# Kernel optimization log

Measured on AMD Instinct MI355X. Metric: run time of the kernel, lower is better.

The kernel has to match this reference:

```python
import jax, jax.numpy as jnp
import numpy as np

N_NODES = 50000
N_EDGES = 1_600_000
D = 64


def setup_inputs() -> dict:
    key = jax.random.key(0)
    k1, k2, k3, k4 = jax.random.split(key, 4)
    x = jax.random.normal(k1, (N_NODES, D), dtype=jnp.float32)
    # Glorot-ish scale for the dense transform
    weight = jax.random.normal(k2, (D, D), dtype=jnp.float32) * (1.0 / np.sqrt(D))
    bias = jnp.zeros((D,), dtype=jnp.float32)
    src = jax.random.randint(k3, (N_EDGES,), 0, N_NODES, dtype=jnp.int32)
    dst = jax.random.randint(k4, (N_EDGES,), 0, N_NODES, dtype=jnp.int32)
    t = jnp.zeros((1,), dtype=jnp.float32)
    return {"t": t, "x": x, "weight": weight, "bias": bias, "src": src, "dst": dst}


def reference(t, x, weight, bias, src, dst):
    # GCDEFunc.forward(t, x) -> GCNLayer(x); dropout=0 (eval / ODE solve).
    n = x.shape[0]
    # symmetric GCN normalization: 1/sqrt(in_degree), 0 for isolated nodes
    deg = jax.ops.segment_sum(jnp.ones_like(dst, dtype=x.dtype), dst, num_segments=n)
    norm = jnp.where(deg > 0, jax.lax.rsqrt(jnp.maximum(deg, 1.0)), 0.0)[:, None]  # [N,1]
    h = x @ weight                 # [N,D] dense transform
    h = h * norm                   # src-side normalization
    # SpMM: sum messages copy_src(h) over incoming edges
    h = jax.ops.segment_sum(h[src], dst, num_segments=n)  # [N,D]
    h = h * norm + bias            # dst-side normalization + bias
    return jax.nn.softplus(h)      # smooth activation for ODE dynamics
```

## Files before the change

### kernel.cpp

```cpp
#include <hip/hip_runtime.h>
#include <hip/hip_fp16.h>

constexpr int N = 50000;
constexpr int D = 64;
constexpr int E = 1600000;
constexpr int NBUCK = (N + 127) / 128;
constexpr int CAP = 4608;
constexpr int BTHREADS = 512;
constexpr int BBLOCKS = 512;
constexpr int EPB = E / BBLOCKS;
constexpr int CPT = (EPB + BTHREADS - 1) / BTHREADS;

__global__ void k_init(int* __restrict__ cursor) {
    int t = threadIdx.x;
    if (t < NBUCK) cursor[t] = t * CAP;
}

__global__ void k_bucket(const int* __restrict__ src, const int* __restrict__ dst,
                         int* __restrict__ cursor, unsigned* __restrict__ packed) {
    __shared__ int lh[NBUCK];
    __shared__ int scanI[NBUCK];
    __shared__ int wsum[8];
    __shared__ int lb[NBUCK];
    __shared__ unsigned stage[EPB];
    int tid = threadIdx.x;
    if (tid < NBUCK) lh[tid] = 0;
    __syncthreads();
    int base_e = blockIdx.x * EPB;
    unsigned pk[CPT];
    int bn[CPT], rk[CPT];
#pragma unroll
    for (int i = 0; i < CPT; ++i) {
        int idx = i * BTHREADS + tid;
        if (idx < EPB) {
            int e = base_e + idx;
            int d = dst[e];
            int s = src[e];
            bn[i] = d >> 7;
            pk[i] = ((unsigned)d << 16) | (unsigned)s;
            rk[i] = atomicAdd(&lh[bn[i]], 1);
        } else bn[i] = -1;
    }
    __syncthreads();
    int w = tid >> 6, l = tid & 63;
    int v = (tid < NBUCK) ? lh[tid] : 0;
    for (int off = 1; off < 64; off <<= 1) {
        int t = __shfl_up(v, off, 64);
        if (l >= off) v += t;
    }
    if (tid < NBUCK) scanI[tid] = v;
    if (l == 63) wsum[w] = v;
    __syncthreads();
    if (tid < 64) {
        int s = (tid < 8) ? wsum[tid] : 0;
        for (int off = 1; off < 8; off <<= 1) {
            int t = __shfl_up(s, off, 64);
            if (tid >= off) s += t;
        }
        if (tid < 8) wsum[tid] = s;
    }
    __syncthreads();
    if (tid < NBUCK && w > 0) scanI[tid] += wsum[w - 1];
    if (tid < NBUCK) {
        int c = lh[tid];
        lb[tid] = c ? atomicAdd(&cursor[tid], c) : 0;
    }
    __syncthreads();
#pragma unroll
    for (int i = 0; i < CPT; ++i) {
        if (bn[i] >= 0) {
            int eb = (bn[i] == 0) ? 0 : scanI[bn[i] - 1];
            stage[eb + rk[i]] = pk[i];
        }
    }
    __syncthreads();
    for (int j = tid; j < EPB; j += BTHREADS) {
        unsigned vv = stage[j];
        int bk = vv >> 23;
        int eb = (bk == 0) ? 0 : scanI[bk - 1];
        packed[lb[bk] + (j - eb)] = vv;
    }
}

__global__ void k_csr(const int* __restrict__ cursor, const unsigned* __restrict__ packed,
                      unsigned short* __restrict__ csr, int* __restrict__ rowptr,
                      int* __restrict__ rowend, float* __restrict__ norm) {
    __shared__ int cnt[128];
    __shared__ int sm[128];
    __shared__ int cur[128];
    __shared__ unsigned short stage[CAP];
    int b = blockIdx.x, tid = threadIdx.x;
    if (tid < 128) cnt[tid] = 0;
    __syncthreads();
    int beg = b * CAP;
    int m = cursor[b] - beg;
    for (int j = tid; j < m; j += 1024)
        atomicAdd(&cnt[(packed[beg + j] >> 16) & 127], 1);
    __syncthreads();
    if (tid < 64) {
        int a = cnt[2 * tid], c1 = cnt[2 * tid + 1];
        int s = a + c1;
        for (int off = 1; off < 64; off <<= 1) {
            int t = __shfl_up(s, off, 64);
            if (tid >= off) s += t;
        }
        sm[2 * tid + 1] = s;
        sm[2 * tid] = s - c1;
    }
    __syncthreads();
    if (tid < 128) {
        int incl = sm[tid];
        int excl = incl - cnt[tid];
        int node = b * 128 + tid;
        if (node < N) {
            rowptr[node] = beg + excl;
            rowend[node] = beg + incl;
            norm[node] = cnt[tid] ? rsqrtf((float)cnt[tid]) : 0.0f;
        }
        cur[tid] = excl;
    }
    __syncthreads();
    for (int j = tid; j < m; j += 1024) {
        unsigned p = packed[beg + j];
        int slot = atomicAdd(&cur[(p >> 16) & 127], 1);
        stage[slot] = (unsigned short)(p & 0xFFFFu);
    }
    __syncthreads();
    unsigned* du = (unsigned*)(csr + beg);
    const unsigned* su = (const unsigned*)stage;
    int mu = m >> 1;
    for (int k = tid; k < mu; k += 1024) du[k] = su[k];
    if ((m & 1) && tid == 0) csr[beg + m - 1] = stage[m - 1];
}

__global__ void k_gemm(const float* __restrict__ x, const float* __restrict__ W,
                       const float* __restrict__ norm, __half* __restrict__ h2) {
    __shared__ float Wl[64 * 64];
    __shared__ float xs[16][64];
    int tid = threadIdx.x;
    const float4* W4 = (const float4*)W;
    float4* Wl4 = (float4*)Wl;
    Wl4[tid] = W4[tid];
    int r = tid >> 6, d = tid & 63;
    int row = blockIdx.x * 16 + r;
    xs[r][d] = x[row * 64 + d];
    __syncthreads();
    float a = 0.0f;
#pragma unroll
    for (int k = 0; k < 64; ++k) a = fmaf(xs[r][k], Wl[k * 64 + d], a);
    h2[row * 64 + d] = __float2half(a * norm[row]);
}

__global__ void k_aggregate(const int* __restrict__ rowptr, const int* __restrict__ rowend,
                            const unsigned short* __restrict__ csr,
                            const __half* __restrict__ h2, const float* __restrict__ norm,
                            const float* __restrict__ bias, float* __restrict__ out) {
    int node = blockIdx.x * 4 + (threadIdx.x >> 6);
    int lane = threadIdx.x & 63;
    int half = lane >> 5;
    int fl = lane & 31;
    const __half2* h2v = (const __half2*)h2;
    int beg = rowptr[node];
    int end = rowend[node];
    int deg = end - beg;
    int myidx = (beg + lane < end) ? (int)csr[beg + lane] : 0;
    int window = deg < 64 ? deg : 64;
    int npair = window >> 1;
    float ax = 0.0f, ay = 0.0f, bx = 0.0f, by = 0.0f;
    int p = 0;
    for (; p + 3 < npair; p += 4) {
        int s0 = __shfl(myidx, 2 * p + half, 64);
        int s1 = __shfl(myidx, 2 * p + 2 + half, 64);
        int s2 = __shfl(myidx, 2 * p + 4 + half, 64);
        int s3 = __shfl(myidx, 2 * p + 6 + half, 64);
        float2 v0 = __half22float2(h2v[s0 * 32 + fl]);
        float2 v1 = __half22float2(h2v[s1 * 32 + fl]);
        float2 v2 = __half22float2(h2v[s2 * 32 + fl]);
        float2 v3 = __half22float2(h2v[s3 * 32 + fl]);
        ax += v0.x + v2.x;  ay += v0.y + v2.y;
        bx += v1.x + v3.x;  by += v1.y + v3.y;
    }
    for (; p < npair; ++p) {
        int s = __shfl(myidx, 2 * p + half, 64);
        float2 v = __half22float2(h2v[s * 32 + fl]);
        ax += v.x;  ay += v.y;
    }
    if (window & 1) {
        int s = __shfl(myidx, window - 1, 64);
        float2 v = __half22float2(h2v[s * 32 + fl]);
        if (half == 0) { ax += v.x;  ay += v.y; }
    }
    if (deg > 64) {
        int j = beg + 64;
        for (; j + 1 < end; j += 2) {
            int s = csr[j + half];
            float2 v = __half22float2(h2v[s * 32 + fl]);
            ax += v.x;  ay += v.y;
        }
        if (j < end) {
            int s = csr[j];
            float2 v = __half22float2(h2v[s * 32 + fl]);
            if (half == 0) { ax += v.x;  ay += v.y; }
        }
    }
    ax += bx;  ay += by;
    ax += __shfl_xor(ax, 32, 64);
    ay += __shfl_xor(ay, 32, 64);
    if (half == 0) {
        float nrm = norm[node];
        float2 bs = ((const float2*)bias)[fl];
        float vx = ax * nrm + bs.x;
        float vy = ay * nrm + bs.y;
        float2 o;
        o.x = fmaxf(vx, 0.0f) + log1pf(expf(-fabsf(vx)));
        o.y = fmaxf(vy, 0.0f) + log1pf(expf(-fabsf(vy)));
        ((float2*)out)[node * 32 + fl] = o;
    }
}

extern "C" void kernel_launch(void* const* d_in, const int* in_sizes, int n_in,
                              void* d_out, int out_size, void* d_ws, size_t ws_size,
                              hipStream_t stream) {
    const float* x    = (const float*)d_in[1];
    const float* W    = (const float*)d_in[2];
    const float* bias = (const float*)d_in[3];
    const int* src = (const int*)d_in[4];
    const int* dst = (const int*)d_in[5];
    float* out = (float*)d_out;

    char* ws = (char*)d_ws;
    __half*         h2     = (__half*)(ws);
    unsigned*       packed = (unsigned*)(ws + 6400000);
    unsigned short* csr    = (unsigned short*)(ws + 13606912);
    int*            rowptr = (int*)(ws + 17210368);
    int*            rowend = (int*)(ws + 17410368);
    float*          norm   = (float*)(ws + 17610368);
    int*            cursor = (int*)(ws + 17810368);

    k_init     <<<1, 512, 0, stream>>>(cursor);
    k_bucket   <<<BBLOCKS, BTHREADS, 0, stream>>>(src, dst, cursor, packed);
    k_csr      <<<NBUCK, 1024, 0, stream>>>(cursor, packed, csr, rowptr, rowend, norm);
    k_gemm     <<<(N + 15) / 16, 1024, 0, stream>>>(x, W, norm, h2);
    k_aggregate<<<(N + 3) / 4, 256, 0, stream>>>(rowptr, rowend, csr, h2, norm, bias, out);
}
```

Measured before the change: 161.5 us.

## Replace init kernel with memset, persistent GEMM blocks, deeper gather unroll

The cursor initialization kernel is replaced by a memset, with bucket offsets made relative so the base is added in the bucket kernel. The GEMM becomes a grid-stride loop over 256 blocks, so W is loaded into shared memory once per block instead of once per 16 rows. The aggregation loop is unrolled to eight gathers per iteration to put more loads in flight. These are three unrelated tweaks. The memset may cost about as much as the tiny kernel it replaces, and fewer GEMM blocks lowers parallelism.

```diff
diff --git a/kernel.cpp b/kernel.cpp
--- a/kernel.cpp
+++ b/kernel.cpp
@@ -10,11 +10,6 @@
 constexpr int BBLOCKS = 512;
 constexpr int EPB = E / BBLOCKS;
 constexpr int CPT = (EPB + BTHREADS - 1) / BTHREADS;
-
-__global__ void k_init(int* __restrict__ cursor) {
-    int t = threadIdx.x;
-    if (t < NBUCK) cursor[t] = t * CAP;
-}
 
 __global__ void k_bucket(const int* __restrict__ src, const int* __restrict__ dst,
                          int* __restrict__ cursor, unsigned* __restrict__ packed) {
@@ -63,7 +58,7 @@
     if (tid < NBUCK && w > 0) scanI[tid] += wsum[w - 1];
     if (tid < NBUCK) {
         int c = lh[tid];
-        lb[tid] = c ? atomicAdd(&cursor[tid], c) : 0;
+        lb[tid] = tid * CAP + (c ? atomicAdd(&cursor[tid], c) : 0);
     }
     __syncthreads();
 #pragma unroll
@@ -93,7 +88,7 @@
     if (tid < 128) cnt[tid] = 0;
     __syncthreads();
     int beg = b * CAP;
-    int m = cursor[b] - beg;
+    int m = cursor[b];
     for (int j = tid; j < m; j += 1024)
         atomicAdd(&cnt[(packed[beg + j] >> 16) & 127], 1);
     __syncthreads();
@@ -138,17 +133,18 @@
     __shared__ float Wl[64 * 64];
     __shared__ float xs[16][64];
     int tid = threadIdx.x;
-    const float4* W4 = (const float4*)W;
-    float4* Wl4 = (float4*)Wl;
-    Wl4[tid] = W4[tid];
+    ((float4*)Wl)[tid] = ((const float4*)W)[tid];
     int r = tid >> 6, d = tid & 63;
-    int row = blockIdx.x * 16 + r;
-    xs[r][d] = x[row * 64 + d];
-    __syncthreads();
-    float a = 0.0f;
+    for (int tile = blockIdx.x; tile < N / 16; tile += 256) {
+        int row = tile * 16 + r;
+        __syncthreads();
+        xs[r][d] = x[row * 64 + d];
+        __syncthreads();
+        float a = 0.0f;
 #pragma unroll
-    for (int k = 0; k < 64; ++k) a = fmaf(xs[r][k], Wl[k * 64 + d], a);
-    h2[row * 64 + d] = __float2half(a * norm[row]);
+        for (int k = 0; k < 64; ++k) a = fmaf(xs[r][k], Wl[k * 64 + d], a);
+        h2[row * 64 + d] = __float2half(a * norm[row]);
+    }
 }
 
 __global__ void k_aggregate(const int* __restrict__ rowptr, const int* __restrict__ rowend,
@@ -168,17 +164,25 @@
     int npair = window >> 1;
     float ax = 0.0f, ay = 0.0f, bx = 0.0f, by = 0.0f;
     int p = 0;
-    for (; p + 3 < npair; p += 4) {
+    for (; p + 7 < npair; p += 8) {
         int s0 = __shfl(myidx, 2 * p + half, 64);
         int s1 = __shfl(myidx, 2 * p + 2 + half, 64);
         int s2 = __shfl(myidx, 2 * p + 4 + half, 64);
         int s3 = __shfl(myidx, 2 * p + 6 + half, 64);
+        int s4 = __shfl(myidx, 2 * p + 8 + half, 64);
+        int s5 = __shfl(myidx, 2 * p + 10 + half, 64);
+        int s6 = __shfl(myidx, 2 * p + 12 + half, 64);
+        int s7 = __shfl(myidx, 2 * p + 14 + half, 64);
         float2 v0 = __half22float2(h2v[s0 * 32 + fl]);
         float2 v1 = __half22float2(h2v[s1 * 32 + fl]);
         float2 v2 = __half22float2(h2v[s2 * 32 + fl]);
         float2 v3 = __half22float2(h2v[s3 * 32 + fl]);
-        ax += v0.x + v2.x;  ay += v0.y + v2.y;
-        bx += v1.x + v3.x;  by += v1.y + v3.y;
+        float2 v4 = __half22float2(h2v[s4 * 32 + fl]);
+        float2 v5 = __half22float2(h2v[s5 * 32 + fl]);
+        float2 v6 = __half22float2(h2v[s6 * 32 + fl]);
+        float2 v7 = __half22float2(h2v[s7 * 32 + fl]);
+        ax += v0.x + v2.x + v4.x + v6.x;  ay += v0.y + v2.y + v4.y + v6.y;
+        bx += v1.x + v3.x + v5.x + v7.x;  by += v1.y + v3.y + v5.y + v7.y;
     }
     for (; p < npair; ++p) {
         int s = __shfl(myidx, 2 * p + half, 64);
@@ -237,9 +241,9 @@
     float*          norm   = (float*)(ws + 17610368);
     int*            cursor = (int*)(ws + 17810368);
 
-    k_init     <<<1, 512, 0, stream>>>(cursor);
+    hipMemsetAsync(cursor, 0, NBUCK * sizeof(int), stream);
     k_bucket   <<<BBLOCKS, BTHREADS, 0, stream>>>(src, dst, cursor, packed);
     k_csr      <<<NBUCK, 1024, 0, stream>>>(cursor, packed, csr, rowptr, rowend, norm);
-    k_gemm     <<<(N + 15) / 16, 1024, 0, stream>>>(x, W, norm, h2);
+    k_gemm     <<<256, 1024, 0, stream>>>(x, W, norm, h2);
     k_aggregate<<<(N + 3) / 4, 256, 0, stream>>>(rowptr, rowend, csr, h2, norm, bias, out);
 }
```

After: 167.0 us. 1.03x slower.
